# Performance work log

Hardware: AMD Instinct MI355X
Metric: run time of the kernel (lower is better)

## Reference

```python
import jax, jax.numpy as jnp
import numpy as np

NUM_STAB = 1e-3  # numerical_stabilizer for relu kernel


def _relu_feature(x, proj):
    # x: [B, L, H, D], proj: [M, D] -> [B, L, H, M]
    ratio = 1.0 / jnp.sqrt(jnp.asarray(proj.shape[0], x.dtype))
    return jax.nn.relu(ratio * jnp.einsum('blhd,md->blhm', x, proj)) + NUM_STAB


def setup_inputs() -> dict:
    key = jax.random.key(0)
    k1, k2, k3, k4, k5 = jax.random.split(key, 5)
    B, L, H, D, M = 16, 576, 12, 64, 8  # L = length_of_side**2 = 24**2
    return {
        'query': jax.random.normal(k1, (B, L, H, D), dtype=jnp.float32),
        'key': jax.random.normal(k2, (B, L, H, D), dtype=jnp.float32),
        'value': jax.random.normal(k3, (B, L, H, D), dtype=jnp.float32),
        'projection_matrix': jax.random.normal(k4, (M, D), dtype=jnp.float32),
        # RPE mask is nonnegative per-head mixing matrix [H, L, L]
        'mask_matrix': jax.random.uniform(k5, (H, L, L), dtype=jnp.float32),
    }


def reference(query, key, value, projection_matrix, mask_matrix):
    # ReLU kernel features (projection_matrix_type='relu')
    q_prime = _relu_feature(query, projection_matrix)  # [B, L, H, M]
    k_prime = _relu_feature(key, projection_matrix)    # [B, L, H, M]
    B, L, H, M = k_prime.shape
    D = value.shape[-1]

    # D_1[b,l,h,m,d] = k'[b,l,h,m] * v[b,l,h,d], flattened over (m,d)
    D_1 = jnp.einsum('blhm,blhd->blhmd', k_prime, value).reshape(B, L, H, M * D)
    # mask-matrix causal/RPE mixing over the L dimension (per head)
    D_1_hat = jnp.einsum('hij,bjhc->bihc', mask_matrix, D_1).reshape(B, L, H, M, D)
    D_2_hat = jnp.einsum('hij,bjhm->bihm', mask_matrix, k_prime)  # [B, L, H, M]

    av_attention = jnp.einsum('blhm,blhmd->blhd', q_prime, D_1_hat)  # [B, L, H, D]
    ks_sum = jnp.sum(D_2_hat, axis=1)                                # [B, H, M]
    normalizer = jnp.einsum('blhm,bhm->blh', q_prime, ks_sum)        # [B, L, H]
    return av_attention / normalizer[..., None]
```

## Files before the change

kernel.cpp:

```cpp
#include <hip/hip_runtime.h>
#include <hip/hip_bf16.h>


#define B_ 16
#define L_ 576
#define H_ 12
#define D_ 64
#define M_ 8
#define NUM_STAB 1e-3f
#define RATIO 0.35355339059327373f

typedef __attribute__((ext_vector_type(8))) short short8;
typedef __attribute__((ext_vector_type(4))) float f32x4;

union Pack {
    uint4 u4;
    short8 s8;
    uint2 u2[2];
    unsigned u[4];
    unsigned short us[8];
};

__device__ inline unsigned short f2bf(float x) {
    union { float f; unsigned u; } a; a.f = x;
    unsigned r = (a.u + 0x7FFFu + ((a.u >> 16) & 1u)) >> 16;
    return (unsigned short)r;
}
__device__ inline unsigned pk2(float lo, float hi) {
    __hip_bfloat162 h = __float22bfloat162_rn(make_float2(lo, hi));
    union { __hip_bfloat162 b; unsigned u; } c; c.b = h;
    return c.u;
}
__device__ inline float bf2f(unsigned short u) {
    union { unsigned u; float f; } c; c.u = (unsigned)u << 16; return c.f;
}

#define WS_W_OFF  (H_ * L_)
#define WS_QP_OFF (H_ * L_ + B_ * H_ * M_)
#define QP_ELEMS  ((size_t)B_ * H_ * L_ * M_)

__global__ __launch_bounds__(256) void feat_kernel(const float* __restrict__ q,
                                                   const float* __restrict__ k,
                                                   const float* __restrict__ proj,
                                                   const float* __restrict__ mask,
                                                   unsigned short* __restrict__ qp,
                                                   unsigned short* __restrict__ kp,
                                                   float* __restrict__ cmask) {
    __shared__ float cred[4][16];
    const int lc = blockIdx.x, h = blockIdx.y, b = blockIdx.z, t = threadIdx.x;
    const int wv = t >> 6, l = t & 63, r8 = l >> 3, c8 = l & 7;
    const int row = lc * 32 + wv * 8 + r8;

    float4 pj0[8], pj1[8];
#pragma unroll
    for (int m = 0; m < 8; ++m) {
        pj0[m] = *(const float4*)(proj + m * 64 + c8 * 8);
        pj1[m] = *(const float4*)(proj + m * 64 + c8 * 8 + 4);
    }

#pragma unroll
    for (int s = 0; s < 2; ++s) {
        const float* src = s ? k : q;
        unsigned short* dst = s ? kp : qp;
        const float* xp = src + (((size_t)b * L_ + row) * H_ + h) * D_ + c8 * 8;
        float4 x0 = *(const float4*)xp;
        float4 x1 = *(const float4*)(xp + 4);
        x0.x *= RATIO; x0.y *= RATIO; x0.z *= RATIO; x0.w *= RATIO;
        x1.x *= RATIO; x1.y *= RATIO; x1.z *= RATIO; x1.w *= RATIO;
        float p[8];
#pragma unroll
        for (int m = 0; m < 8; ++m) {
            p[m] = x0.x * pj0[m].x + x0.y * pj0[m].y + x0.z * pj0[m].z + x0.w * pj0[m].w
                 + x1.x * pj1[m].x + x1.y * pj1[m].y + x1.z * pj1[m].z + x1.w * pj1[m].w;
        }
#pragma unroll
        for (int st = 1; st <= 4; st <<= 1) {
#pragma unroll
            for (int m = 0; m < 8; ++m) p[m] += __shfl_xor(p[m], st, 64);
        }
        float r = p[0];
        r = (c8 == 1) ? p[1] : r;
        r = (c8 == 2) ? p[2] : r;
        r = (c8 == 3) ? p[3] : r;
        r = (c8 == 4) ? p[4] : r;
        r = (c8 == 5) ? p[5] : r;
        r = (c8 == 6) ? p[6] : r;
        r = (c8 == 7) ? p[7] : r;
        r = fmaxf(r, 0.f) + NUM_STAB;
        dst[((size_t)(b * H_ + h) * L_ + row) * 8 + c8] = f2bf(r);
    }

    if (b < 2) {
        const int c = t & 15, rg = t >> 4;
        const int col0 = lc * 32 + b * 16;
        const float* mb = mask + (size_t)h * L_ * L_ + col0 + c;
        float a = 0.f;
#pragma unroll 4
        for (int k2 = 0; k2 < 36; ++k2) a += mb[(size_t)(rg + 16 * k2) * L_];
        a += __shfl_xor(a, 16, 64);
        a += __shfl_xor(a, 32, 64);
        if ((l >> 4) == 0) cred[wv][c] = a;
        __syncthreads();
        if (t < 16) cmask[h * L_ + col0 + t] = cred[0][t] + cred[1][t] + cred[2][t] + cred[3][t];
    }
}

__global__ __launch_bounds__(64) void wsum_kernel(const unsigned short* __restrict__ kp,
                                                  const float* __restrict__ cmask,
                                                  float* __restrict__ wbuf) {
    const int bh = blockIdx.x, lx = threadIdx.x;
    const int h = bh % H_;
    const unsigned short* kpb = kp + (size_t)bh * L_ * 8;
    const float* cm = cmask + h * L_;
    float a[8] = {0.f, 0.f, 0.f, 0.f, 0.f, 0.f, 0.f, 0.f};
    for (int j = lx; j < L_; j += 64) {
        const float c = cm[j];
        Pack pk; pk.u4 = *(const uint4*)(kpb + (size_t)j * 8);
#pragma unroll
        for (int m = 0; m < 8; ++m) a[m] += c * bf2f(pk.us[m]);
    }
#pragma unroll
    for (int st = 1; st < 64; st <<= 1) {
#pragma unroll
        for (int m = 0; m < 8; ++m) a[m] += __shfl_xor(a[m], st, 64);
    }
    float r = a[0];
    r = (lx == 1) ? a[1] : r;
    r = (lx == 2) ? a[2] : r;
    r = (lx == 3) ? a[3] : r;
    r = (lx == 4) ? a[4] : r;
    r = (lx == 5) ? a[5] : r;
    r = (lx == 6) ? a[6] : r;
    r = (lx == 7) ? a[7] : r;
    if (lx < 8) wbuf[(size_t)bh * 8 + lx] = r;
}

__global__ __launch_bounds__(256, 4) void attn_kernel(const float* __restrict__ v,
                                                      const float* __restrict__ mask,
                                                      const unsigned short* __restrict__ qp,
                                                      const unsigned short* __restrict__ kp,
                                                      const float* __restrict__ wbuf,
                                                      float* __restrict__ out) {
    __shared__ __align__(16) unsigned short Sp[2][4][16 * 64];

    const int t = threadIdx.x;
    int id = blockIdx.x;
    const int bhi = id & 7; id >>= 3;
    const int blo = id & 1; id >>= 1;
    const int it = id % 9, h = id / 9;
    const int b = bhi * 2 + blo;
    const int i0 = it * 64;

    const int wv = t >> 6, l = t & 63, c15 = l & 15, kq = l >> 4;
    const int sxor = (c15 & 7) << 4;

    const float* maskbase = mask + (size_t)h * L_ * L_ + (size_t)(i0 + 16 * wv + c15) * L_ + 4 * kq;
    const unsigned short* kpb = kp + (size_t)(b * H_ + h) * L_ * 8;
    const float* vbase = v + ((size_t)b * L_ * H_ + h) * D_ + 16 * wv + c15;

    short8 Bq;
    {
        Pack pk; pk.u4 = make_uint4(0, 0, 0, 0);
        if (kq == 0)
            pk.u4 = *(const uint4*)(qp + ((size_t)(b * H_ + h) * L_ + i0 + 16 * wv + c15) * 8);
        Bq = pk.s8;
    }

    f32x4 acc0 = {0.f, 0.f, 0.f, 0.f}, acc1 = acc0, acc2 = acc0, acc3 = acc0;
    const f32x4 zz = {0.f, 0.f, 0.f, 0.f};

    uint4 a0 = make_uint4(0, 0, 0, 0), a1 = a0, a2 = a0, a3 = a0;
    float4 mv0, mv1, mv2, mv3;
    float vf0[8], vf1[8];

    if (kq == 0) {
        a0 = *(const uint4*)(kpb + (size_t)(c15) * 8);
        a1 = *(const uint4*)(kpb + (size_t)(16 + c15) * 8);
        a2 = *(const uint4*)(kpb + (size_t)(32 + c15) * 8);
        a3 = *(const uint4*)(kpb + (size_t)(48 + c15) * 8);
    }
    mv0 = *(const float4*)(maskbase + 0);
    mv1 = *(const float4*)(maskbase + 16);
    mv2 = *(const float4*)(maskbase + 32);
    mv3 = *(const float4*)(maskbase + 48);
#pragma unroll
    for (int e = 0; e < 8; ++e) vf0[e] = vbase[(size_t)(kq * 8 + e) * (H_ * D_)];
#pragma unroll
    for (int e = 0; e < 8; ++e) vf1[e] = vbase[(size_t)(32 + kq * 8 + e) * (H_ * D_)];

    for (int jt = 0; jt < 9; ++jt) {
        const int slab = jt & 1;
        char* SpW = (char*)Sp[slab][wv];

        f32x4 s0, s1, s2, s3;
        {
            Pack p0, p1, p2, p3;
            p0.u4 = a0; p1.u4 = a1; p2.u4 = a2; p3.u4 = a3;
            s0 = __builtin_amdgcn_mfma_f32_16x16x32_bf16(p0.s8, Bq, zz, 0, 0, 0);
            s1 = __builtin_amdgcn_mfma_f32_16x16x32_bf16(p1.s8, Bq, zz, 0, 0, 0);
            s2 = __builtin_amdgcn_mfma_f32_16x16x32_bf16(p2.s8, Bq, zz, 0, 0, 0);
            s3 = __builtin_amdgcn_mfma_f32_16x16x32_bf16(p3.s8, Bq, zz, 0, 0, 0);
        }

        {
            const int sb = c15 * 128 + 8 * kq;
            uint2 st2;
            st2.x = pk2(s0[0] * mv0.x, s0[1] * mv0.y);
            st2.y = pk2(s0[2] * mv0.z, s0[3] * mv0.w);
            *(uint2*)(SpW + ((sb + 0) ^ sxor)) = st2;
            st2.x = pk2(s1[0] * mv1.x, s1[1] * mv1.y);
            st2.y = pk2(s1[2] * mv1.z, s1[3] * mv1.w);
            *(uint2*)(SpW + ((sb + 32) ^ sxor)) = st2;
            st2.x = pk2(s2[0] * mv2.x, s2[1] * mv2.y);
            st2.y = pk2(s2[2] * mv2.z, s2[3] * mv2.w);
            *(uint2*)(SpW + ((sb + 64) ^ sxor)) = st2;
            st2.x = pk2(s3[0] * mv3.x, s3[1] * mv3.y);
            st2.y = pk2(s3[2] * mv3.z, s3[3] * mv3.w);
            *(uint2*)(SpW + ((sb + 96) ^ sxor)) = st2;
        }

        Pack bv0, bv1;
#pragma unroll
        for (int q4 = 0; q4 < 4; ++q4) bv0.u[q4] = pk2(vf0[2 * q4], vf0[2 * q4 + 1]);
#pragma unroll
        for (int q4 = 0; q4 < 4; ++q4) bv1.u[q4] = pk2(vf1[2 * q4], vf1[2 * q4 + 1]);

        asm volatile("s_waitcnt lgkmcnt(0)\n\ts_barrier" ::: "memory");

        {
            const int j0n = ((jt < 8) ? jt + 1 : 0) * 64;
            if (kq == 0) {
                a0 = *(const uint4*)(kpb + (size_t)(j0n + c15) * 8);
                a1 = *(const uint4*)(kpb + (size_t)(j0n + 16 + c15) * 8);
                a2 = *(const uint4*)(kpb + (size_t)(j0n + 32 + c15) * 8);
                a3 = *(const uint4*)(kpb + (size_t)(j0n + 48 + c15) * 8);
            }
            mv0 = *(const float4*)(maskbase + j0n + 0);
            mv1 = *(const float4*)(maskbase + j0n + 16);
            mv2 = *(const float4*)(maskbase + j0n + 32);
            mv3 = *(const float4*)(maskbase + j0n + 48);
#pragma unroll
            for (int e = 0; e < 8; ++e) vf0[e] = vbase[(size_t)(j0n + kq * 8 + e) * (H_ * D_)];
#pragma unroll
            for (int e = 0; e < 8; ++e) vf1[e] = vbase[(size_t)(j0n + 32 + kq * 8 + e) * (H_ * D_)];
        }

        {
            const char* SpR = (const char*)Sp[slab][0];
            const int rb = c15 * 128;
#pragma unroll
            for (int iw = 0; iw < 4; ++iw) {
                const char* ch = SpR + iw * 2048;
                short8 As0 = *(const short8*)(ch + ((rb + 16 * kq) ^ sxor));
                short8 As1 = *(const short8*)(ch + ((rb + 64 + 16 * kq) ^ sxor));
                f32x4* ap = (iw == 0) ? &acc0 : (iw == 1) ? &acc1 : (iw == 2) ? &acc2 : &acc3;
                *ap = __builtin_amdgcn_mfma_f32_16x16x32_bf16(As0, bv0.s8, *ap, 0, 0, 0);
                *ap = __builtin_amdgcn_mfma_f32_16x16x32_bf16(As1, bv1.s8, *ap, 0, 0, 0);
            }
        }
    }

    const float* wp = wbuf + (size_t)(b * H_ + h) * 8;
    const float4 w0 = *(const float4*)wp;
    const float4 w1 = *(const float4*)(wp + 4);
    const f32x4 aa[4] = {acc0, acc1, acc2, acc3};
#pragma unroll
    for (int iw = 0; iw < 4; ++iw) {
        Pack pq;
        pq.u4 = *(const uint4*)(qp + ((size_t)(b * H_ + h) * L_ + i0 + 16 * iw + c15) * 8);
        float n = bf2f(pq.us[0]) * w0.x + bf2f(pq.us[1]) * w0.y +
                  bf2f(pq.us[2]) * w0.z + bf2f(pq.us[3]) * w0.w +
                  bf2f(pq.us[4]) * w1.x + bf2f(pq.us[5]) * w1.y +
                  bf2f(pq.us[6]) * w1.z + bf2f(pq.us[7]) * w1.w;
        float* ob = out + (((size_t)b * L_ + i0 + 16 * iw) * H_ + h) * D_ + 16 * wv + c15;
#pragma unroll
        for (int r = 0; r < 4; ++r) {
            float iv = 1.0f / __shfl(n, 4 * kq + r, 64);
            ob[(size_t)(4 * kq + r) * (H_ * D_)] = aa[iw][r] * iv;
        }
    }
}

extern "C" void kernel_launch(void* const* d_in, const int* in_sizes, int n_in,
                              void* d_out, int out_size, void* d_ws, size_t ws_size,
                              hipStream_t stream) {
    const float* q    = (const float*)d_in[0];
    const float* k    = (const float*)d_in[1];
    const float* v    = (const float*)d_in[2];
    const float* proj = (const float*)d_in[3];
    const float* mask = (const float*)d_in[4];
    float* out = (float*)d_out;

    float* ws = (float*)d_ws;
    float* cmask = ws;
    float* wbuf  = ws + WS_W_OFF;
    unsigned short* qp_w = (unsigned short*)(ws + WS_QP_OFF);
    unsigned short* kp_w = qp_w + QP_ELEMS;

    feat_kernel<<<dim3(L_ / 32, H_, B_), 256, 0, stream>>>(q, k, proj, mask, qp_w, kp_w, cmask);
    wsum_kernel<<<B_ * H_, 64, 0, stream>>>(kp_w, cmask, wbuf);
    attn_kernel<<<1728, 256, 0, stream>>>(v, mask, qp_w, kp_w, wbuf, out);
}
```

Before: 188.1 us.

## Prefetch mask tiles two iterations ahead, unroll loop, remap block order for XCDs

Mask tiles are now double-buffered in registers and loaded two j-tiles ahead instead of one, and the j-loop is fully unrolled so the buffer indices are compile-time constants. The block index mapping is also changed to spread consecutive block IDs across 8 groups (XCD-style interleave), keeping blocks that share a head and row tile on the same die for L2 reuse of the mask. These aim to hide global latency on the mask stream and improve cache locality, at the cost of more registers, which may hurt the 4-blocks-per-SM occupancy target.

Measured after the change: 188.8 us. About the same (+0.4%).

```diff
diff --git a/kernel.cpp b/kernel.cpp
--- a/kernel.cpp
+++ b/kernel.cpp
@@ -144,11 +144,11 @@
     __shared__ __align__(16) unsigned short Sp[2][4][16 * 64];
 
     const int t = threadIdx.x;
-    int id = blockIdx.x;
-    const int bhi = id & 7; id >>= 3;
-    const int blo = id & 1; id >>= 1;
-    const int it = id % 9, h = id / 9;
-    const int b = bhi * 2 + blo;
+    const int n = blockIdx.x;
+    const int vid = (n & 7) * 216 + (n >> 3);
+    const int b = vid & 15;
+    const int g = vid >> 4;
+    const int it = g % 9, h = g / 9;
     const int i0 = it * 64;
 
     const int wv = t >> 6, l = t & 63, c15 = l & 15, kq = l >> 4;
@@ -170,8 +170,8 @@
     const f32x4 zz = {0.f, 0.f, 0.f, 0.f};
 
     uint4 a0 = make_uint4(0, 0, 0, 0), a1 = a0, a2 = a0, a3 = a0;
-    float4 mv0, mv1, mv2, mv3;
     float vf0[8], vf1[8];
+    float4 mvb[2][4];
 
     if (kq == 0) {
         a0 = *(const uint4*)(kpb + (size_t)(c15) * 8);
@@ -179,15 +179,16 @@
         a2 = *(const uint4*)(kpb + (size_t)(32 + c15) * 8);
         a3 = *(const uint4*)(kpb + (size_t)(48 + c15) * 8);
     }
-    mv0 = *(const float4*)(maskbase + 0);
-    mv1 = *(const float4*)(maskbase + 16);
-    mv2 = *(const float4*)(maskbase + 32);
-    mv3 = *(const float4*)(maskbase + 48);
 #pragma unroll
     for (int e = 0; e < 8; ++e) vf0[e] = vbase[(size_t)(kq * 8 + e) * (H_ * D_)];
 #pragma unroll
     for (int e = 0; e < 8; ++e) vf1[e] = vbase[(size_t)(32 + kq * 8 + e) * (H_ * D_)];
-
+#pragma unroll
+    for (int T = 0; T < 4; ++T) mvb[0][T] = *(const float4*)(maskbase + 16 * T);
+#pragma unroll
+    for (int T = 0; T < 4; ++T) mvb[1][T] = *(const float4*)(maskbase + 64 + 16 * T);
+
+#pragma unroll
     for (int jt = 0; jt < 9; ++jt) {
         const int slab = jt & 1;
         char* SpW = (char*)Sp[slab][wv];
@@ -203,19 +204,21 @@
         }
 
         {
+            const float4 m0 = mvb[jt & 1][0], m1 = mvb[jt & 1][1];
+            const float4 m2 = mvb[jt & 1][2], m3 = mvb[jt & 1][3];
             const int sb = c15 * 128 + 8 * kq;
             uint2 st2;
-            st2.x = pk2(s0[0] * mv0.x, s0[1] * mv0.y);
-            st2.y = pk2(s0[2] * mv0.z, s0[3] * mv0.w);
+            st2.x = pk2(s0[0] * m0.x, s0[1] * m0.y);
+            st2.y = pk2(s0[2] * m0.z, s0[3] * m0.w);
             *(uint2*)(SpW + ((sb + 0) ^ sxor)) = st2;
-            st2.x = pk2(s1[0] * mv1.x, s1[1] * mv1.y);
-            st2.y = pk2(s1[2] * mv1.z, s1[3] * mv1.w);
+            st2.x = pk2(s1[0] * m1.x, s1[1] * m1.y);
+            st2.y = pk2(s1[2] * m1.z, s1[3] * m1.w);
             *(uint2*)(SpW + ((sb + 32) ^ sxor)) = st2;
-            st2.x = pk2(s2[0] * mv2.x, s2[1] * mv2.y);
-            st2.y = pk2(s2[2] * mv2.z, s2[3] * mv2.w);
+            st2.x = pk2(s2[0] * m2.x, s2[1] * m2.y);
+            st2.y = pk2(s2[2] * m2.z, s2[3] * m2.w);
             *(uint2*)(SpW + ((sb + 64) ^ sxor)) = st2;
-            st2.x = pk2(s3[0] * mv3.x, s3[1] * mv3.y);
-            st2.y = pk2(s3[2] * mv3.z, s3[3] * mv3.w);
+            st2.x = pk2(s3[0] * m3.x, s3[1] * m3.y);
+            st2.y = pk2(s3[2] * m3.z, s3[3] * m3.w);
             *(uint2*)(SpW + ((sb + 96) ^ sxor)) = st2;
         }
 
@@ -228,21 +231,20 @@
         asm volatile("s_waitcnt lgkmcnt(0)\n\ts_barrier" ::: "memory");
 
         {
-            const int j0n = ((jt < 8) ? jt + 1 : 0) * 64;
+            const int j1 = ((jt < 8) ? jt + 1 : 0) * 64;
+            const int j2 = ((jt < 7) ? jt + 2 : 0) * 64;
             if (kq == 0) {
-                a0 = *(const uint4*)(kpb + (size_t)(j0n + c15) * 8);
-                a1 = *(const uint4*)(kpb + (size_t)(j0n + 16 + c15) * 8);
-                a2 = *(const uint4*)(kpb + (size_t)(j0n + 32 + c15) * 8);
-                a3 = *(const uint4*)(kpb + (size_t)(j0n + 48 + c15) * 8);
+                a0 = *(const uint4*)(kpb + (size_t)(j1 + c15) * 8);
+                a1 = *(const uint4*)(kpb + (size_t)(j1 + 16 + c15) * 8);
+                a2 = *(const uint4*)(kpb + (size_t)(j1 + 32 + c15) * 8);
+                a3 = *(const uint4*)(kpb + (size_t)(j1 + 48 + c15) * 8);
             }
-            mv0 = *(const float4*)(maskbase + j0n + 0);
-            mv1 = *(const float4*)(maskbase + j0n + 16);
-            mv2 = *(const float4*)(maskbase + j0n + 32);
-            mv3 = *(const float4*)(maskbase + j0n + 48);
-#pragma unroll
-            for (int e = 0; e < 8; ++e) vf0[e] = vbase[(size_t)(j0n + kq * 8 + e) * (H_ * D_)];
-#pragma unroll
-            for (int e = 0; e < 8; ++e) vf1[e] = vbase[(size_t)(j0n + 32 + kq * 8 + e) * (H_ * D_)];
+#pragma unroll
+            for (int e = 0; e < 8; ++e) vf0[e] = vbase[(size_t)(j1 + kq * 8 + e) * (H_ * D_)];
+#pragma unroll
+            for (int e = 0; e < 8; ++e) vf1[e] = vbase[(size_t)(j1 + 32 + kq * 8 + e) * (H_ * D_)];
+#pragma unroll
+            for (int T = 0; T < 4; ++T) mvb[jt & 1][T] = *(const float4*)(maskbase + j2 + 16 * T);
         }
 
         {
@@ -268,14 +270,14 @@
     for (int iw = 0; iw < 4; ++iw) {
         Pack pq;
         pq.u4 = *(const uint4*)(qp + ((size_t)(b * H_ + h) * L_ + i0 + 16 * iw + c15) * 8);
-        float n = bf2f(pq.us[0]) * w0.x + bf2f(pq.us[1]) * w0.y +
-                  bf2f(pq.us[2]) * w0.z + bf2f(pq.us[3]) * w0.w +
-                  bf2f(pq.us[4]) * w1.x + bf2f(pq.us[5]) * w1.y +
-                  bf2f(pq.us[6]) * w1.z + bf2f(pq.us[7]) * w1.w;
+        float n2 = bf2f(pq.us[0]) * w0.x + bf2f(pq.us[1]) * w0.y +
+                   bf2f(pq.us[2]) * w0.z + bf2f(pq.us[3]) * w0.w +
+                   bf2f(pq.us[4]) * w1.x + bf2f(pq.us[5]) * w1.y +
+                   bf2f(pq.us[6]) * w1.z + bf2f(pq.us[7]) * w1.w;
         float* ob = out + (((size_t)b * L_ + i0 + 16 * iw) * H_ + h) * D_ + 16 * wv + c15;
 #pragma unroll
         for (int r = 0; r < 4; ++r) {
-            float iv = 1.0f / __shfl(n, 4 * kq + r, 64);
+            float iv = 1.0f / __shfl(n2, 4 * kq + r, 64);
             ob[(size_t)(4 * kq + r) * (H_ * D_)] = aa[iw][r] * iv;
         }
     }
```
